# Optimization experiments

Hardware: AMD Instinct MI355X
Metric: run time of the kernel (lower is better)

The kernel has to match this reference:

```python
import jax, jax.numpy as jnp
import numpy as np

N = 50000
E = 500000
D_IN = 128
D_HID = 128  # hidden_channels; conv1 outputs 2*D_HID


def setup_inputs() -> dict:
    key = jax.random.key(0)
    ks = jax.random.split(key, 8)
    x = jax.random.normal(ks[0], (N, D_IN), dtype=jnp.float32)
    edge_index = jax.random.randint(ks[1], (2, E), 0, N, dtype=jnp.int64)
    # Glorot-ish init for weights, zeros for biases (PyG GCNConv default style)
    W1 = jax.random.normal(ks[2], (D_IN, 2 * D_HID), dtype=jnp.float32) / np.sqrt(D_IN)
    b1 = jnp.zeros((2 * D_HID,), dtype=jnp.float32)
    W2 = jax.random.normal(ks[3], (2 * D_HID, D_HID), dtype=jnp.float32) / np.sqrt(2 * D_HID)
    b2 = jnp.zeros((D_HID,), dtype=jnp.float32)
    Wfc = jax.random.normal(ks[4], (D_HID, 6), dtype=jnp.float32) / np.sqrt(D_HID)
    bfc = jnp.zeros((6,), dtype=jnp.float32)
    return {"x": x, "W1": W1, "b1": b1, "W2": W2, "b2": b2,
            "Wfc": Wfc, "bfc": bfc, "edge_index": edge_index}


def _gcn_conv(x, W, b, src, dst, deg_isqrt, n):
    # PyG GCNConv: h = W x; out_i = sum_j norm_ij * h_j + b, with self-loops
    h = x @ W                                  # [n, d_out]
    norm = deg_isqrt[src] * deg_isqrt[dst]     # [E+n]
    msg = h[src] * norm[:, None]               # gather + scale
    out = jax.ops.segment_sum(msg, dst, num_segments=n)  # scatter-add
    return out + b


def reference(x, W1, b1, W2, b2, Wfc, bfc, edge_index):
    n = x.shape[0]
    loop = jnp.arange(n, dtype=edge_index.dtype)
    src = jnp.concatenate([edge_index[0], loop])  # add self-loops
    dst = jnp.concatenate([edge_index[1], loop])
    deg = jax.ops.segment_sum(jnp.ones_like(dst, dtype=x.dtype), dst, num_segments=n)
    deg_isqrt = jnp.where(deg > 0, jax.lax.rsqrt(jnp.maximum(deg, 1e-12)), 0.0)
    h = jax.nn.relu(_gcn_conv(x, W1, b1, src, dst, deg_isqrt, n))
    h = jax.nn.relu(_gcn_conv(h, W2, b2, src, dst, deg_isqrt, n))
    return h @ Wfc + bfc
```

## Files before the change

kernel.cpp:

```cpp
#include <hip/hip_runtime.h>


typedef _Float16 f16;
typedef __attribute__((ext_vector_type(8))) _Float16 f16x8;
typedef __attribute__((ext_vector_type(4))) float f32x4;

#define GLOAD16(g, l)                                                      \
    __builtin_amdgcn_global_load_lds(                                      \
        (const __attribute__((address_space(1))) void*)(g),                \
        (__attribute__((address_space(3))) void*)(l), 16, 0, 0)

__global__ void count_wt_kernel(const int* __restrict__ dst, int* __restrict__ cnt,
                                int e,
                                const float* __restrict__ W1, f16* __restrict__ wt1,
                                const float* __restrict__ W2, f16* __restrict__ wt2) {
    int b = blockIdx.x;
    if (b < 128) {
        int j = b * 256 + threadIdx.x;
        int nn = j >> 7, k = j & 127;
        wt1[j] = (f16)W1[(long long)k * 256 + nn];
    } else if (b < 256) {
        int j = (b - 128) * 256 + threadIdx.x;
        int nn = j >> 8, k = j & 255;
        wt2[j] = (f16)W2[(long long)k * 128 + nn];
    } else {
        for (int i = (b - 256) * 256 + (int)threadIdx.x; i < e; i += 2048 * 256)
            atomicAdd(&cnt[dst[i]], 1);
    }
}

__global__ void scan1_kernel(const int* __restrict__ cnt, int* __restrict__ local,
                             int* __restrict__ partials, float* __restrict__ disq,
                             int n) {
    __shared__ int lds[256];
    int base = blockIdx.x * 1024;
    int t = threadIdx.x;
    int v[4];
    int sum = 0;
    #pragma unroll
    for (int j = 0; j < 4; j++) {
        int i = base + t * 4 + j;
        v[j] = (i < n) ? cnt[i] : 0;
        if (i < n) disq[i] = rsqrtf(1.0f + (float)v[j]);
        sum += v[j];
    }
    lds[t] = sum;
    __syncthreads();
    for (int off = 1; off < 256; off <<= 1) {
        int x = (t >= off) ? lds[t - off] : 0;
        __syncthreads();
        lds[t] += x;
        __syncthreads();
    }
    int excl = lds[t] - sum;
    if (t == 255) partials[blockIdx.x] = lds[255];
    int run = excl;
    #pragma unroll
    for (int j = 0; j < 4; j++) {
        int i = base + t * 4 + j;
        if (i < n) local[i] = run;
        run += v[j];
    }
}

__global__ void scan2_kernel(int* __restrict__ partials, int nb) {
    __shared__ int lds[1024];
    int t = threadIdx.x;
    int v = (t < nb) ? partials[t] : 0;
    lds[t] = v;
    __syncthreads();
    for (int off = 1; off < 1024; off <<= 1) {
        int x = (t >= off) ? lds[t - off] : 0;
        __syncthreads();
        lds[t] += x;
        __syncthreads();
    }
    if (t < nb) partials[t] = lds[t] - v;
}

__global__ void scan3_xs_kernel(const int* __restrict__ local,
                                const int* __restrict__ partials,
                                int* __restrict__ row_ptr, int* __restrict__ cursor,
                                int n, int e_total, int nb,
                                const float4* __restrict__ x,
                                const float* __restrict__ disq,
                                f16* __restrict__ xs, long long n4) {
    int b = blockIdx.x;
    int t = threadIdx.x;
    if (b < nb) {
        int base = b * 1024;
        int add = partials[b];
        #pragma unroll
        for (int j = 0; j < 4; j++) {
            int i = base + t * 4 + j;
            if (i < n) {
                int p = local[i] + add;
                row_ptr[i] = p;
                cursor[i] = p;
            }
        }
        if (b == 0 && t == 0) row_ptr[n] = e_total;
        return;
    }
    long long i = (long long)(b - nb) * 256 + t;
    if (i < n4) {
        float4 v = x[i];
        float s = disq[i >> 5];
        union { f16 h[4]; short4 s4; } u;
        u.h[0] = (f16)(v.x * s); u.h[1] = (f16)(v.y * s);
        u.h[2] = (f16)(v.z * s); u.h[3] = (f16)(v.w * s);
        *(short4*)(xs + i * 4) = u.s4;
    }
}

__global__ void csr_fill_kernel(const int* __restrict__ src, const int* __restrict__ dst,
                                int* __restrict__ cursor, int* __restrict__ esorted,
                                int e) {
    for (int i = blockIdx.x * blockDim.x + threadIdx.x; i < e;
         i += gridDim.x * blockDim.x) {
        int d = dst[i];
        int pos = atomicAdd(&cursor[d], 1);
        esorted[pos] = src[i];
    }
}

template <int MODE>
__global__ __launch_bounds__(256)
void gemm_f16_kernel(const f16* __restrict__ A,
                     const f16* __restrict__ Bt,
                     f16* __restrict__ C,
                     const float* __restrict__ rowscale,
                     const float* __restrict__ bias,
                     int M, int K, int Nc) {
    __shared__ __align__(16) char smem[2 * 32 * 1024];
    const int tid = threadIdx.x;
    const int lane = tid & 63;
    const int wid = tid >> 6;
    const int wr = wid >> 1;
    const int wc = wid & 1;
    const int row0 = blockIdx.y * 128;
    const int col0 = blockIdx.x * 128;
    const bool rows_full = (row0 + 128 <= M);

    f32x4 acc[4][4];
    #pragma unroll
    for (int mr = 0; mr < 4; mr++)
        #pragma unroll
        for (int nr = 0; nr < 4; nr++)
            acc[mr][nr] = (f32x4){0.f, 0.f, 0.f, 0.f};

    auto stage = [&](int buf, int k0) {
        char* as = smem + buf * (32 * 1024);
        char* bs = as + 16 * 1024;
        if (rows_full) {
            #pragma unroll
            for (int i = 0; i < 4; i++) {
                int flat = i * 256 + tid;
                int r = flat >> 3, gp = flat & 7;
                int g = gp ^ (r & 7);
                const f16* src = A + (long long)(row0 + r) * K + k0 + g * 8;
                GLOAD16(src, as + (i * 256 + wid * 64) * 16);
            }
        } else {
            #pragma unroll
            for (int i = 0; i < 4; i++) {
                int flat = i * 256 + tid;
                int r = flat >> 3, gp = flat & 7;
                int g = gp ^ (r & 7);
                int gr = row0 + r;
                float4 v = {0.f, 0.f, 0.f, 0.f};
                if (gr < M) v = *(const float4*)(A + (long long)gr * K + k0 + g * 8);
                *(float4*)(as + flat * 16) = v;
            }
        }
        #pragma unroll
        for (int i = 0; i < 4; i++) {
            int flat = i * 256 + tid;
            int nn = flat >> 3, gp = flat & 7;
            int g = gp ^ (nn & 7);
            const f16* src = Bt + (long long)(col0 + nn) * K + k0 + g * 8;
            GLOAD16(src, bs + (i * 256 + wid * 64) * 16);
        }
    };

    auto compute = [&](int buf) {
        char* as = smem + buf * (32 * 1024);
        char* bs = as + 16 * 1024;
        #pragma unroll
        for (int ks = 0; ks < 2; ks++) {
            const int kb = (ks * 32 + ((lane >> 4) * 8)) * 2;
            f16x8 af[4], bf[4];
            #pragma unroll
            for (int mr = 0; mr < 4; mr++) {
                int r = wr * 64 + mr * 16 + (lane & 15);
                af[mr] = *(const f16x8*)(as + r * 128 + (kb ^ ((r & 7) << 4)));
            }
            #pragma unroll
            for (int nr = 0; nr < 4; nr++) {
                int c = wc * 64 + nr * 16 + (lane & 15);
                bf[nr] = *(const f16x8*)(bs + c * 128 + (kb ^ ((c & 7) << 4)));
            }
            #pragma unroll
            for (int mr = 0; mr < 4; mr++)
                #pragma unroll
                for (int nr = 0; nr < 4; nr++)
                    acc[mr][nr] = __builtin_amdgcn_mfma_f32_16x16x32_f16(
                        af[mr], bf[nr], acc[mr][nr], 0, 0, 0);
        }
    };

    const int nt = K >> 6;
    stage(0, 0);
    __syncthreads();
    int cur = 0;
    for (int t = 0; t < nt; t++) {
        if (t + 1 < nt) stage(cur ^ 1, (t + 1) * 64);
        compute(cur);
        __syncthreads();
        cur ^= 1;
    }

    float bv[4] = {0.f, 0.f, 0.f, 0.f};
    if (MODE == 1) {
        #pragma unroll
        for (int nr = 0; nr < 4; nr++)
            bv[nr] = bias[col0 + wc * 64 + nr * 16 + (lane & 15)];
    }
    #pragma unroll
    for (int mr = 0; mr < 4; mr++) {
        #pragma unroll
        for (int reg = 0; reg < 4; reg++) {
            int row = row0 + wr * 64 + mr * 16 + (lane >> 4) * 4 + reg;
            if (row < M) {
                float s = rowscale[row];
                int col = col0 + wc * 64 + (lane & 15);
                #pragma unroll
                for (int nr = 0; nr < 4; nr++) {
                    float v = acc[mr][nr][reg] * s;
                    if (MODE == 1) v = fmaxf(v + bv[nr], 0.0f);
                    C[(long long)row * Nc + col + nr * 16] = (f16)v;
                }
            }
        }
    }
}

__global__ void gather_sum_f16_kernel(const float4* __restrict__ h,
                                      float4* __restrict__ out,
                                      const int* __restrict__ row_ptr,
                                      const int* __restrict__ esorted, int n) {
    int lane = threadIdx.x & 63;
    long long wave = (blockIdx.x * (long long)blockDim.x + threadIdx.x) >> 6;
    int sub = lane >> 4;
    int sl = lane & 15;
    long long node = wave * 4 + sub;
    if (node >= n) return;
    int beg = row_ptr[node], end = row_ptr[node + 1];
    float acc[8];
    {
        float4 v = h[node * 16 + sl];
        const f16* hp = (const f16*)&v;
        #pragma unroll
        for (int j = 0; j < 8; j++) acc[j] = (float)hp[j];
    }
    int e = beg;
    for (; e + 8 <= end; e += 8) {
        int s[8];
        #pragma unroll
        for (int u = 0; u < 8; u++) s[u] = esorted[e + u];
        float4 v[8];
        #pragma unroll
        for (int u = 0; u < 8; u++) v[u] = h[(long long)s[u] * 16 + sl];
        #pragma unroll
        for (int u = 0; u < 8; u++) {
            const f16* p = (const f16*)&v[u];
            #pragma unroll
            for (int j = 0; j < 8; j++) acc[j] += (float)p[j];
        }
    }
    for (; e < end; e++) {
        int s = esorted[e];
        float4 v = h[(long long)s * 16 + sl];
        const f16* hp = (const f16*)&v;
        #pragma unroll
        for (int j = 0; j < 8; j++) acc[j] += (float)hp[j];
    }
    union { float4 f4; f16 hh[8]; } o;
    #pragma unroll
    for (int j = 0; j < 8; j++) o.hh[j] = (f16)acc[j];
    out[node * 16 + sl] = o.f4;
}

__global__ void gather_fc_kernel(const float4* __restrict__ t,
                                 const int* __restrict__ row_ptr,
                                 const int* __restrict__ esorted,
                                 const float* __restrict__ disq,
                                 const float* __restrict__ b2,
                                 const float* __restrict__ Wfc,
                                 const float* __restrict__ bfc,
                                 float* __restrict__ out, int n) {
    __shared__ float wf[6 * 132];
    for (int i = threadIdx.x; i < 6 * 128; i += 256) {
        int k = i >> 7, ch = i & 127;
        wf[k * 132 + ch] = Wfc[ch * 6 + k];
    }
    __syncthreads();
    int lane = threadIdx.x & 63;
    long long wave = (blockIdx.x * (long long)blockDim.x + threadIdx.x) >> 6;
    int sub = lane >> 4;
    int sl = lane & 15;
    long long node = wave * 4 + sub;
    if (node >= n) return;
    int beg = row_ptr[node], end = row_ptr[node + 1];
    float acc[8];
    {
        float4 v = t[node * 16 + sl];
        const f16* hp = (const f16*)&v;
        #pragma unroll
        for (int j = 0; j < 8; j++) acc[j] = (float)hp[j];
    }
    int e = beg;
    for (; e + 8 <= end; e += 8) {
        int s[8];
        #pragma unroll
        for (int u = 0; u < 8; u++) s[u] = esorted[e + u];
        float4 v[8];
        #pragma unroll
        for (int u = 0; u < 8; u++) v[u] = t[(long long)s[u] * 16 + sl];
        #pragma unroll
        for (int u = 0; u < 8; u++) {
            const f16* p = (const f16*)&v[u];
            #pragma unroll
            for (int j = 0; j < 8; j++) acc[j] += (float)p[j];
        }
    }
    for (; e < end; e++) {
        int s = esorted[e];
        float4 v = t[(long long)s * 16 + sl];
        const f16* hp = (const f16*)&v;
        #pragma unroll
        for (int j = 0; j < 8; j++) acc[j] += (float)hp[j];
    }
    float sc = disq[node];
    const float4* b4 = (const float4*)(b2 + sl * 8);
    float4 bb0 = b4[0], bb1 = b4[1];
    float bb[8] = {bb0.x, bb0.y, bb0.z, bb0.w, bb1.x, bb1.y, bb1.z, bb1.w};
    float h2[8];
    #pragma unroll
    for (int j = 0; j < 8; j++)
        h2[j] = fmaxf(fmaf(acc[j], sc, bb[j]), 0.0f);
    float p[6];
    #pragma unroll
    for (int k = 0; k < 6; k++) {
        float s = 0.f;
        #pragma unroll
        for (int j = 0; j < 8; j++) s += h2[j] * wf[k * 132 + sl * 8 + j];
        p[k] = s;
    }
    #pragma unroll
    for (int off = 8; off >= 1; off >>= 1)
        #pragma unroll
        for (int k = 0; k < 6; k++) p[k] += __shfl_down(p[k], off);
    if (sl == 0) {
        #pragma unroll
        for (int k = 0; k < 6; k++)
            out[(long long)node * 6 + k] = p[k] + bfc[k];
    }
}

extern "C" void kernel_launch(void* const* d_in, const int* in_sizes, int n_in,
                              void* d_out, int out_size, void* d_ws, size_t ws_size,
                              hipStream_t stream) {
    const float* x   = (const float*)d_in[0];
    const float* W1  = (const float*)d_in[1];
    const float* b1  = (const float*)d_in[2];
    const float* W2  = (const float*)d_in[3];
    const float* b2  = (const float*)d_in[4];
    const float* Wfc = (const float*)d_in[5];
    const float* bfc = (const float*)d_in[6];
    const int* edges = (const int*)d_in[7];

    const int N = in_sizes[0] / 128;
    const int E = in_sizes[7] / 2;
    const int* e_src = edges;
    const int* e_dst = edges + E;

    char* ws = (char*)d_ws;
    size_t off = 0;
    auto alloc = [&](size_t bytes) {
        void* p = ws + off;
        off += (bytes + 255) & ~(size_t)255;
        return p;
    };
    const int NB = (N + 1023) / 1024;
    float* disq     = (float*)alloc((size_t)N * 4);
    int*   cnt      = (int*)  alloc((size_t)N * 4);
    int*   slocal   = (int*)  alloc((size_t)N * 4);
    int*   partials = (int*)  alloc((size_t)NB * 4);
    int*   row_ptr  = (int*)  alloc((size_t)(N + 1) * 4);
    int*   cursor   = (int*)  alloc((size_t)N * 4);
    int*   esorted  = (int*)  alloc((size_t)E * 4);
    f16*   xs       = (f16*)  alloc((size_t)N * 128 * 2);
    f16*   wt1      = (f16*)  alloc((size_t)256 * 128 * 2);
    f16*   wt2      = (f16*)  alloc((size_t)128 * 256 * 2);
    f16*   agg1     = (f16*)  alloc((size_t)N * 128 * 2);
    f16*   h1       = (f16*)  alloc((size_t)N * 256 * 2);
    f16*   tbuf     = (f16*)  alloc((size_t)N * 128 * 2);
    (void)ws_size; (void)n_in;

    float* out = (float*)d_out; (void)out_size;

    hipMemsetAsync(cnt, 0, (size_t)N * sizeof(int), stream);
    count_wt_kernel<<<256 + 2048, 256, 0, stream>>>(e_dst, cnt, E,
                                                    W1, wt1, W2, wt2);
    scan1_kernel<<<NB, 256, 0, stream>>>(cnt, slocal, partials, disq, N);
    scan2_kernel<<<1, 1024, 0, stream>>>(partials, NB);
    {
        long long n4 = (long long)N * 128 / 4;
        int xb = (int)((n4 + 255) / 256);
        scan3_xs_kernel<<<NB + xb, 256, 0, stream>>>(
            slocal, partials, row_ptr, cursor, N, E, NB,
            (const float4*)x, disq, xs, n4);
    }
    csr_fill_kernel<<<2048, 256, 0, stream>>>(e_src, e_dst, cursor, esorted, E);

    {
        long long waves = ((long long)N + 3) / 4;
        int blocks = (int)((waves + 3) / 4);
        gather_sum_f16_kernel<<<blocks, 256, 0, stream>>>(
            (const float4*)xs, (float4*)agg1, row_ptr, esorted, N);
    }
    {
        dim3 g(256 / 128, (N + 127) / 128);
        gemm_f16_kernel<1><<<g, 256, 0, stream>>>(agg1, wt1, h1, disq, b1,
                                                  N, 128, 256);
    }

    {
        dim3 g(128 / 128, (N + 127) / 128);
        gemm_f16_kernel<0><<<g, 256, 0, stream>>>(h1, wt2, tbuf, disq, nullptr,
                                                  N, 256, 128);
    }
    {
        long long waves = ((long long)N + 3) / 4;
        int blocks = (int)((waves + 3) / 4);
        gather_fc_kernel<<<blocks, 256, 0, stream>>>(
            (const float4*)tbuf, row_ptr, esorted, disq, b2, Wfc, bfc, out, N);
    }
}
```

Before: 229.1 us.

## Fuse CSR build, scans and prep into one cooperative kernel with grid syncs

Replaces the memset plus five separate preprocessing launches (count, three scan stages, CSR fill, weight transpose, x scaling) with a single cooperative kernel of 1024 blocks that separates phases with grid.sync(). The aim is to remove per-kernel launch gaps and drain overheads in the small, latency-bound preprocessing stages. In exchange, grid-wide barriers carry their own cost, and the phases now run on a fixed grid that must fit co-resident, which can reduce parallelism for the edge-atomic phases. The second-level scan now uses a 256-thread block, which assumes NB (49) is at most 256.

```diff
diff --git a/kernel.cpp b/kernel.cpp
--- a/kernel.cpp
+++ b/kernel.cpp
@@ -1,4 +1,7 @@
 #include <hip/hip_runtime.h>
+#include <hip/hip_cooperative_groups.h>
+
+namespace cg = cooperative_groups;
 
 
 typedef _Float16 f16;
@@ -10,100 +13,97 @@
         (const __attribute__((address_space(1))) void*)(g),                \
         (__attribute__((address_space(3))) void*)(l), 16, 0, 0)
 
-__global__ void count_wt_kernel(const int* __restrict__ dst, int* __restrict__ cnt,
-                                int e,
-                                const float* __restrict__ W1, f16* __restrict__ wt1,
-                                const float* __restrict__ W2, f16* __restrict__ wt2) {
-    int b = blockIdx.x;
-    if (b < 128) {
-        int j = b * 256 + threadIdx.x;
+__global__ void __launch_bounds__(256)
+csr_build_kernel(const int* __restrict__ src, const int* __restrict__ dst,
+                 int* __restrict__ cnt, int* __restrict__ slocal,
+                 int* __restrict__ partials, int* __restrict__ row_ptr,
+                 int* __restrict__ cursor, int* __restrict__ esorted,
+                 float* __restrict__ disq,
+                 const float* __restrict__ W1, f16* __restrict__ wt1,
+                 const float* __restrict__ W2, f16* __restrict__ wt2,
+                 const float4* __restrict__ x, f16* __restrict__ xs,
+                 int n, int e, int nblk, long long n4) {
+    cg::grid_group grid = cg::this_grid();
+    const int tid = threadIdx.x;
+    const int b = blockIdx.x;
+    const int gsz = gridDim.x * 256;
+    const int gid = b * 256 + tid;
+    __shared__ int lds[256];
+
+    for (int i = gid; i < n; i += gsz) cnt[i] = 0;
+    for (int j = gid; j < 32768; j += gsz) {
         int nn = j >> 7, k = j & 127;
         wt1[j] = (f16)W1[(long long)k * 256 + nn];
-    } else if (b < 256) {
-        int j = (b - 128) * 256 + threadIdx.x;
+    }
+    for (int j = gid; j < 32768; j += gsz) {
         int nn = j >> 8, k = j & 255;
         wt2[j] = (f16)W2[(long long)k * 128 + nn];
-    } else {
-        for (int i = (b - 256) * 256 + (int)threadIdx.x; i < e; i += 2048 * 256)
-            atomicAdd(&cnt[dst[i]], 1);
-    }
-}
-
-__global__ void scan1_kernel(const int* __restrict__ cnt, int* __restrict__ local,
-                             int* __restrict__ partials, float* __restrict__ disq,
-                             int n) {
-    __shared__ int lds[256];
-    int base = blockIdx.x * 1024;
-    int t = threadIdx.x;
-    int v[4];
-    int sum = 0;
-    #pragma unroll
-    for (int j = 0; j < 4; j++) {
-        int i = base + t * 4 + j;
-        v[j] = (i < n) ? cnt[i] : 0;
-        if (i < n) disq[i] = rsqrtf(1.0f + (float)v[j]);
-        sum += v[j];
-    }
-    lds[t] = sum;
-    __syncthreads();
-    for (int off = 1; off < 256; off <<= 1) {
-        int x = (t >= off) ? lds[t - off] : 0;
+    }
+    grid.sync();
+
+    for (int i = gid; i < e; i += gsz) atomicAdd(&cnt[dst[i]], 1);
+    grid.sync();
+
+    if (b < nblk) {
+        int base = b * 1024;
+        int v[4];
+        int sum = 0;
+        #pragma unroll
+        for (int j = 0; j < 4; j++) {
+            int i = base + tid * 4 + j;
+            v[j] = (i < n) ? cnt[i] : 0;
+            if (i < n) disq[i] = rsqrtf(1.0f + (float)v[j]);
+            sum += v[j];
+        }
+        lds[tid] = sum;
         __syncthreads();
-        lds[t] += x;
+        for (int off = 1; off < 256; off <<= 1) {
+            int t = (tid >= off) ? lds[tid - off] : 0;
+            __syncthreads();
+            lds[tid] += t;
+            __syncthreads();
+        }
+        int excl = lds[tid] - sum;
+        if (tid == 255) partials[b] = lds[255];
+        int run = excl;
+        #pragma unroll
+        for (int j = 0; j < 4; j++) {
+            int i = base + tid * 4 + j;
+            if (i < n) slocal[i] = run;
+            run += v[j];
+        }
+    }
+    grid.sync();
+
+    if (b == 0) {
+        int v = (tid < nblk) ? partials[tid] : 0;
+        lds[tid] = v;
         __syncthreads();
-    }
-    int excl = lds[t] - sum;
-    if (t == 255) partials[blockIdx.x] = lds[255];
-    int run = excl;
-    #pragma unroll
-    for (int j = 0; j < 4; j++) {
-        int i = base + t * 4 + j;
-        if (i < n) local[i] = run;
-        run += v[j];
-    }
-}
-
-__global__ void scan2_kernel(int* __restrict__ partials, int nb) {
-    __shared__ int lds[1024];
-    int t = threadIdx.x;
-    int v = (t < nb) ? partials[t] : 0;
-    lds[t] = v;
-    __syncthreads();
-    for (int off = 1; off < 1024; off <<= 1) {
-        int x = (t >= off) ? lds[t - off] : 0;
-        __syncthreads();
-        lds[t] += x;
-        __syncthreads();
-    }
-    if (t < nb) partials[t] = lds[t] - v;
-}
-
-__global__ void scan3_xs_kernel(const int* __restrict__ local,
-                                const int* __restrict__ partials,
-                                int* __restrict__ row_ptr, int* __restrict__ cursor,
-                                int n, int e_total, int nb,
-                                const float4* __restrict__ x,
-                                const float* __restrict__ disq,
-                                f16* __restrict__ xs, long long n4) {
-    int b = blockIdx.x;
-    int t = threadIdx.x;
-    if (b < nb) {
+        for (int off = 1; off < 256; off <<= 1) {
+            int t = (tid >= off) ? lds[tid - off] : 0;
+            __syncthreads();
+            lds[tid] += t;
+            __syncthreads();
+        }
+        if (tid < nblk) partials[tid] = lds[tid] - v;
+    }
+    grid.sync();
+
+    if (b < nblk) {
         int base = b * 1024;
         int add = partials[b];
         #pragma unroll
         for (int j = 0; j < 4; j++) {
-            int i = base + t * 4 + j;
+            int i = base + tid * 4 + j;
             if (i < n) {
-                int p = local[i] + add;
+                int p = slocal[i] + add;
                 row_ptr[i] = p;
                 cursor[i] = p;
             }
         }
-        if (b == 0 && t == 0) row_ptr[n] = e_total;
-        return;
-    }
-    long long i = (long long)(b - nb) * 256 + t;
-    if (i < n4) {
+        if (b == 0 && tid == 0) row_ptr[n] = e;
+    }
+    for (long long i = gid; i < n4; i += gsz) {
         float4 v = x[i];
         float s = disq[i >> 5];
         union { f16 h[4]; short4 s4; } u;
@@ -111,13 +111,9 @@
         u.h[2] = (f16)(v.z * s); u.h[3] = (f16)(v.w * s);
         *(short4*)(xs + i * 4) = u.s4;
     }
-}
-
-__global__ void csr_fill_kernel(const int* __restrict__ src, const int* __restrict__ dst,
-                                int* __restrict__ cursor, int* __restrict__ esorted,
-                                int e) {
-    for (int i = blockIdx.x * blockDim.x + threadIdx.x; i < e;
-         i += gridDim.x * blockDim.x) {
+    grid.sync();
+
+    for (int i = gid; i < e; i += gsz) {
         int d = dst[i];
         int pos = atomicAdd(&cursor[d], 1);
         esorted[pos] = src[i];
@@ -410,19 +406,19 @@
 
     float* out = (float*)d_out; (void)out_size;
 
-    hipMemsetAsync(cnt, 0, (size_t)N * sizeof(int), stream);
-    count_wt_kernel<<<256 + 2048, 256, 0, stream>>>(e_dst, cnt, E,
-                                                    W1, wt1, W2, wt2);
-    scan1_kernel<<<NB, 256, 0, stream>>>(cnt, slocal, partials, disq, N);
-    scan2_kernel<<<1, 1024, 0, stream>>>(partials, NB);
     {
         long long n4 = (long long)N * 128 / 4;
-        int xb = (int)((n4 + 255) / 256);
-        scan3_xs_kernel<<<NB + xb, 256, 0, stream>>>(
-            slocal, partials, row_ptr, cursor, N, E, NB,
-            (const float4*)x, disq, xs, n4);
-    }
-    csr_fill_kernel<<<2048, 256, 0, stream>>>(e_src, e_dst, cursor, esorted, E);
+        int nblk = NB;
+        void* args[] = {
+            (void*)&e_src, (void*)&e_dst, (void*)&cnt, (void*)&slocal,
+            (void*)&partials, (void*)&row_ptr, (void*)&cursor, (void*)&esorted,
+            (void*)&disq, (void*)&W1, (void*)&wt1, (void*)&W2, (void*)&wt2,
+            (void*)&x, (void*)&xs, (void*)&N, (void*)&E, (void*)&nblk,
+            (void*)&n4
+        };
+        hipLaunchCooperativeKernel((const void*)csr_build_kernel,
+                                   dim3(1024), dim3(256), args, 0, stream);
+    }
 
     {
         long long waves = ((long long)N + 3) / 4;
```

After: 715.6 us. +212.4%, slower.
